# Kernel optimization log

Hardware: AMD Instinct MI355X
Metric: run time of the kernel (lower is better)

Reference implementation:

```python
import jax, jax.numpy as jnp
import numpy as np

N_NODES = 100000
N_EDGES = 50000   # number of hyperedges
NNZ = 500000      # incidence entries
IN_C = 128
OUT_C = 128


def setup_inputs() -> dict:
    key = jax.random.key(0)
    k1, k2, k3, k4 = jax.random.split(key, 4)
    x = jax.random.normal(k1, (N_NODES, IN_C), dtype=jnp.float32)
    node_idx = jax.random.randint(k2, (NNZ,), 0, N_NODES, dtype=jnp.int32)
    edge_idx = jax.random.randint(k3, (NNZ,), 0, N_EDGES, dtype=jnp.int32)
    hyperedge_index = jnp.stack([node_idx, edge_idx], axis=0)  # [2, NNZ]
    W = jax.random.normal(k4, (IN_C, OUT_C), dtype=jnp.float32) / np.sqrt(IN_C).astype(np.float32)
    b = jnp.zeros((OUT_C,), dtype=jnp.float32)
    return {"x": x, "hyperedge_index": hyperedge_index, "W": W, "b": b}


def reference(x, hyperedge_index, W, b):
    # PyG HypergraphConv (use_attention=False, heads=1, unit hyperedge weights):
    #   out = D^{-1} H B^{-1} H^T (X W) + b
    node_idx = hyperedge_index[0]  # [NNZ] node index of each incidence
    edge_idx = hyperedge_index[1]  # [NNZ] hyperedge index of each incidence

    xw = x @ W  # [N_NODES, OUT_C]

    ones = jnp.ones(node_idx.shape[0], dtype=xw.dtype)
    deg_n = jax.ops.segment_sum(ones, node_idx, num_segments=N_NODES)  # D
    d_inv = jnp.where(deg_n > 0, 1.0 / deg_n, 0.0)
    deg_e = jax.ops.segment_sum(ones, edge_idx, num_segments=N_EDGES)  # B
    b_inv = jnp.where(deg_e > 0, 1.0 / deg_e, 0.0)

    # node -> hyperedge: m_e = B^{-1}_e * sum_{v in e} xw_v
    edge_feat = jax.ops.segment_sum(xw[node_idx], edge_idx, num_segments=N_EDGES)
    edge_feat = edge_feat * b_inv[:, None]  # [N_EDGES, OUT_C]

    # hyperedge -> node: out_v = D^{-1}_v * sum_{e \ni v} m_e
    out = jax.ops.segment_sum(edge_feat[edge_idx], node_idx, num_segments=N_NODES)
    out = out * d_inv[:, None]  # [N_NODES, OUT_C]

    return out + b
```

## Files before the change

### kernel.cpp

```cpp
#include <hip/hip_runtime.h>

typedef unsigned short u16;
typedef unsigned int u32;

#define N_NODES 100000
#define N_EDGES 50000
#define C 128
#define G_GEMM 1563
#define NCNT (N_EDGES + N_NODES)
#define NBUCKC 1172
#define BCHUNK 2048

static __device__ __forceinline__ float bf2f(u16 h) {
    u32 u = ((u32)h) << 16;
    float f;
    __builtin_memcpy(&f, &u, 4);
    return f;
}

static __device__ __forceinline__ u16 f2bf(float f) {
    u32 u;
    __builtin_memcpy(&u, &f, 4);
    return (u16)((u + 0x7fffu + ((u >> 16) & 1u)) >> 16);
}

typedef short s16x8 __attribute__((ext_vector_type(8)));
typedef float f32x4 __attribute__((ext_vector_type(4)));

__global__ void transpose_w(const float* __restrict__ W, u16* __restrict__ Wt) {
    int idx = blockIdx.x * 256 + threadIdx.x;
    int k = idx >> 7, oc = idx & 127;
    Wt[oc * 128 + k] = f2bf(W[k * 128 + oc]);
}

__global__ __launch_bounds__(256) void gemm_k(
    const float* __restrict__ x, const u16* __restrict__ Wt,
    u16* __restrict__ xw) {
    __shared__ __align__(16) float xs[64 * C];
    int tid = threadIdx.x;
    int blk = blockIdx.x;
    int lane = tid & 63;
    int wave = tid >> 6;

    size_t gbase = (size_t)blk * 64 * C;
#pragma unroll
    for (int rnd = 0; rnd < 8; ++rnd) {
        int fl = rnd * 1024 + wave * 256 + lane * 4;
        int grow = blk * 64 + (fl >> 7);
        const float* src = (grow < N_NODES) ? (x + gbase + fl) : x;
        __builtin_amdgcn_global_load_lds(
            (const __attribute__((address_space(1))) void*)src,
            (__attribute__((address_space(3))) void*)(xs + rnd * 1024 + wave * 256),
            16, 0, 0);
    }
    __syncthreads();

    int tile = blk * 4 + wave;
    int m = lane & 15;
    int quad = lane >> 4;
    bool live = (tile < 6250);

    union { uint4 u; s16x8 v; } a[4];
    if (live) {
        const float* xr = xs + (wave * 16 + m) * C + quad * 8;
#pragma unroll
        for (int kk = 0; kk < 4; ++kk) {
            float4 v0 = *(const float4*)(xr + kk * 32);
            float4 v1 = *(const float4*)(xr + kk * 32 + 4);
            a[kk].u.x = (u32)f2bf(v0.x) | ((u32)f2bf(v0.y) << 16);
            a[kk].u.y = (u32)f2bf(v0.z) | ((u32)f2bf(v0.w) << 16);
            a[kk].u.z = (u32)f2bf(v1.x) | ((u32)f2bf(v1.y) << 16);
            a[kk].u.w = (u32)f2bf(v1.z) | ((u32)f2bf(v1.w) << 16);
        }
    }
    __syncthreads();

    u16* ct = (u16*)xs;
    if (live) {
        f32x4 acc[8];
#pragma unroll
        for (int nt = 0; nt < 8; ++nt) acc[nt] = (f32x4){0.f, 0.f, 0.f, 0.f};
#pragma unroll
        for (int kk = 0; kk < 4; ++kk) {
            int kb = kk * 32 + quad * 8;
#pragma unroll
            for (int nt = 0; nt < 8; ++nt) {
                union { uint4 u; s16x8 v; } b;
                b.u = *(const uint4*)(Wt + (size_t)(nt * 16 + m) * C + kb);
                acc[nt] = __builtin_amdgcn_mfma_f32_16x16x32_bf16(a[kk].v, b.v, acc[nt], 0, 0, 0);
            }
        }
#pragma unroll
        for (int nt = 0; nt < 8; ++nt)
#pragma unroll
            for (int r = 0; r < 4; ++r)
                ct[(wave * 16 + quad * 4 + r) * C + nt * 16 + m] = f2bf(acc[nt][r]);
    }
    __syncthreads();

#pragma unroll
    for (int r = 0; r < 4; ++r) {
        int f = r * 2048 + tid * 8;
        int grow = blk * 64 + (f >> 7);
        if (grow < N_NODES)
            *(uint4*)(xw + (size_t)blk * 64 * C + f) = *(const uint4*)(ct + f);
    }
}

__global__ __launch_bounds__(256) void bucket_hist_k(
    const int* __restrict__ ni, const int* __restrict__ ei,
    u32* __restrict__ cntM, int nnz, int nb1) {
    __shared__ u32 h[NBUCKC];
    for (int b = threadIdx.x; b < NBUCKC; b += 256) h[b] = 0;
    __syncthreads();
    int i0 = blockIdx.x * BCHUNK;
    int iend = min(i0 + BCHUNK, nnz);
    for (int i = i0 + threadIdx.x; i < iend; i += 256) {
        int e = ei[i], n = ni[i];
        atomicAdd(&h[e >> 7], 1u);
        atomicAdd(&h[(N_EDGES + n) >> 7], 1u);
    }
    __syncthreads();
    for (int b = threadIdx.x; b < NBUCKC; b += 256)
        cntM[(size_t)b * nb1 + blockIdx.x] = h[b];
}

__global__ __launch_bounds__(256) void scan_a2(const u32* __restrict__ cnt,
                                               u32* __restrict__ off,
                                               u32* __restrict__ bsum, int N) {
    __shared__ u32 wsum[4];
    int tid = threadIdx.x;
    int base = blockIdx.x * 1024 + tid * 4;
    u32 v0 = 0, v1 = 0, v2 = 0, v3 = 0;
    if (base + 3 < N) {
        uint4 v = *(const uint4*)(cnt + base);
        v0 = v.x; v1 = v.y; v2 = v.z; v3 = v.w;
    } else {
        if (base + 0 < N) v0 = cnt[base + 0];
        if (base + 1 < N) v1 = cnt[base + 1];
        if (base + 2 < N) v2 = cnt[base + 2];
        if (base + 3 < N) v3 = cnt[base + 3];
    }
    u32 s = v0 + v1 + v2 + v3;
    int lane = tid & 63, wv = tid >> 6;
    u32 x = s;
    for (int d = 1; d < 64; d <<= 1) {
        u32 y = __shfl_up(x, (unsigned)d);
        if (lane >= d) x += y;
    }
    if (lane == 63) wsum[wv] = x;
    __syncthreads();
    u32 wo = 0;
    for (int w = 0; w < 4; ++w) wo += (w < wv) ? wsum[w] : 0u;
    u32 ex = wo + x - s;
    if (base + 0 < N) off[base + 0] = ex;
    if (base + 1 < N) off[base + 1] = ex + v0;
    if (base + 2 < N) off[base + 2] = ex + v0 + v1;
    if (base + 3 < N) off[base + 3] = ex + v0 + v1 + v2;
    if (tid == 255) bsum[blockIdx.x] = wo + x;
}

__global__ __launch_bounds__(256) void scan_b2(u32* __restrict__ bsum, int nb) {
    __shared__ u32 wsum[4];
    int t = threadIdx.x;
    u32 v0 = (2 * t < nb) ? bsum[2 * t] : 0u;
    u32 v1 = (2 * t + 1 < nb) ? bsum[2 * t + 1] : 0u;
    u32 s = v0 + v1;
    int lane = t & 63, wv = t >> 6;
    u32 x = s;
    for (int d = 1; d < 64; d <<= 1) {
        u32 y = __shfl_up(x, (unsigned)d);
        if (lane >= d) x += y;
    }
    if (lane == 63) wsum[wv] = x;
    __syncthreads();
    u32 wo = 0;
    for (int w = 0; w < 4; ++w) wo += (w < wv) ? wsum[w] : 0u;
    u32 ex = wo + x - s;
    if (2 * t < nb) bsum[2 * t] = ex;
    if (2 * t + 1 < nb) bsum[2 * t + 1] = ex + v0;
}

__global__ __launch_bounds__(256) void bucket_place_k(
    const int* __restrict__ ni, const int* __restrict__ ei,
    const u32* __restrict__ offM, const u32* __restrict__ bsum,
    u32* __restrict__ stage, int nnz, int nb1) {
    __shared__ u32 cur[NBUCKC];
    for (int b = threadIdx.x; b < NBUCKC; b += 256) {
        size_t idx = (size_t)b * nb1 + blockIdx.x;
        cur[b] = offM[idx] + bsum[idx >> 10];
    }
    __syncthreads();
    int i0 = blockIdx.x * BCHUNK;
    int iend = min(i0 + BCHUNK, nnz);
    for (int i = i0 + threadIdx.x; i < iend; i += 256) {
        int e = ei[i], n = ni[i];
        u32 p1 = atomicAdd(&cur[e >> 7], 1u);
        stage[p1] = ((u32)(e & 127) << 17) | (u32)n;
        int k2 = N_EDGES + n;
        u32 p2 = atomicAdd(&cur[k2 >> 7], 1u);
        stage[p2] = ((u32)(k2 & 127) << 17) | (u32)e;
    }
}

__global__ __launch_bounds__(256) void bucket_csr_k(
    const u32* __restrict__ offM, const u32* __restrict__ bsum,
    const u32* __restrict__ stage, u32* __restrict__ csr,
    uint2* __restrict__ rowinfo, int nnz, int nb1) {
    __shared__ u32 h[128];
    __shared__ u32 ks[128];
    int b = blockIdx.x;
    size_t i0 = (size_t)b * nb1;
    u32 gstart = offM[i0] + bsum[i0 >> 10];
    u32 gend;
    if (b + 1 < NBUCKC) {
        size_t i1 = (size_t)(b + 1) * nb1;
        gend = offM[i1] + bsum[i1 >> 10];
    } else {
        gend = (u32)(2 * nnz);
    }
    int size = (int)(gend - gstart);
    if (threadIdx.x < 128) h[threadIdx.x] = 0;
    __syncthreads();
    for (int i = threadIdx.x; i < size; i += 256)
        atomicAdd(&h[stage[gstart + i] >> 17], 1u);
    __syncthreads();
    if (threadIdx.x < 64) {
        int l = threadIdx.x;
        u32 s0 = h[2 * l], s1 = h[2 * l + 1];
        u32 ps = s0 + s1;
        u32 x = ps;
        for (int d = 1; d < 64; d <<= 1) {
            u32 y = __shfl_up(x, (unsigned)d);
            if (l >= d) x += y;
        }
        u32 ex = x - ps;
        ks[2 * l] = ex;
        ks[2 * l + 1] = ex + s0;
        int gk = b * 128 + 2 * l;
        if (gk < NCNT) rowinfo[gk] = make_uint2(gstart + ex, s0);
        if (gk + 1 < NCNT) rowinfo[gk + 1] = make_uint2(gstart + ex + s0, s1);
    }
    __syncthreads();
    for (int i = threadIdx.x; i < size; i += 256) {
        u32 en = stage[gstart + i];
        u32 kl = en >> 17;
        u32 p = atomicAdd(&ks[kl], 1u);
        csr[gstart + p] = en & 0x1FFFFu;
    }
}

#define GATHERP(SRC)                                                          \
    for (u32 base = 0; base < deg; base += 64) {                              \
        int m = (int)min(64u, deg - base);                                    \
        int myidx = (lane < m) ? (int)csr[start + base + lane] : 0;           \
        for (int t = 0; t < m; t += 8) {                                      \
            int e0 = min(t + 0 + half, m - 1), e1 = min(t + 2 + half, m - 1); \
            int e2 = min(t + 4 + half, m - 1), e3 = min(t + 6 + half, m - 1); \
            int r0 = __shfl(myidx, e0), r1 = __shfl(myidx, e1);               \
            int r2 = __shfl(myidx, e2), r3 = __shfl(myidx, e3);               \
            uint2 u0 = ((const uint2*)(SRC + (size_t)r0 * C))[ch];            \
            uint2 u1 = ((const uint2*)(SRC + (size_t)r1 * C))[ch];            \
            uint2 u2 = ((const uint2*)(SRC + (size_t)r2 * C))[ch];            \
            uint2 u3 = ((const uint2*)(SRC + (size_t)r3 * C))[ch];            \
            float m0 = (t + 0 + half < m) ? 1.f : 0.f;                        \
            float m1 = (t + 2 + half < m) ? 1.f : 0.f;                        \
            float m2 = (t + 4 + half < m) ? 1.f : 0.f;                        \
            float m3 = (t + 6 + half < m) ? 1.f : 0.f;                        \
            a0 += m0 * bf2f((u16)(u0.x & 0xffffu)) + m1 * bf2f((u16)(u1.x & 0xffffu)) \
                + m2 * bf2f((u16)(u2.x & 0xffffu)) + m3 * bf2f((u16)(u3.x & 0xffffu)); \
            a1 += m0 * bf2f((u16)(u0.x >> 16)) + m1 * bf2f((u16)(u1.x >> 16)) \
                + m2 * bf2f((u16)(u2.x >> 16)) + m3 * bf2f((u16)(u3.x >> 16)); \
            a2 += m0 * bf2f((u16)(u0.y & 0xffffu)) + m1 * bf2f((u16)(u1.y & 0xffffu)) \
                + m2 * bf2f((u16)(u2.y & 0xffffu)) + m3 * bf2f((u16)(u3.y & 0xffffu)); \
            a3 += m0 * bf2f((u16)(u0.y >> 16)) + m1 * bf2f((u16)(u1.y >> 16)) \
                + m2 * bf2f((u16)(u2.y >> 16)) + m3 * bf2f((u16)(u3.y >> 16)); \
        }                                                                     \
    }                                                                         \
    a0 += __shfl_xor(a0, 32);                                                 \
    a1 += __shfl_xor(a1, 32);                                                 \
    a2 += __shfl_xor(a2, 32);                                                 \
    a3 += __shfl_xor(a3, 32);

__global__ __launch_bounds__(256) void edge_gather_k(const u16* __restrict__ xw,
                                                     const uint2* __restrict__ rowinfo,
                                                     const u32* __restrict__ csrC,
                                                     u16* __restrict__ ef) {
    int e = blockIdx.x * 4 + (threadIdx.x >> 6);
    if (e >= N_EDGES) return;
    int lane = threadIdx.x & 63;
    int half = lane >> 5, ch = lane & 31;
    uint2 ri = rowinfo[e];
    u32 deg = ri.y;
    u32 start = ri.x;
    const u32* csr = csrC;
    float a0 = 0.f, a1 = 0.f, a2 = 0.f, a3 = 0.f;
    GATHERP(xw)
    float sc = deg ? 1.f / (float)deg : 0.f;
    if (lane < 32) {
        uint2 w;
        w.x = (u32)f2bf(a0 * sc) | ((u32)f2bf(a1 * sc) << 16);
        w.y = (u32)f2bf(a2 * sc) | ((u32)f2bf(a3 * sc) << 16);
        ((uint2*)(ef + (size_t)e * C))[ch] = w;
    }
}

__global__ __launch_bounds__(256) void node_gather_k(const u16* __restrict__ ef,
                                                     const uint2* __restrict__ rowinfo,
                                                     const u32* __restrict__ csrC,
                                                     const float* __restrict__ bias,
                                                     float* __restrict__ out) {
    int v = blockIdx.x * 4 + (threadIdx.x >> 6);
    if (v >= N_NODES) return;
    int lane = threadIdx.x & 63;
    int half = lane >> 5, ch = lane & 31;
    uint2 ri = rowinfo[N_EDGES + v];
    u32 deg = ri.y;
    u32 start = ri.x;
    const u32* csr = csrC;
    float a0 = 0.f, a1 = 0.f, a2 = 0.f, a3 = 0.f;
    GATHERP(ef)
    float sc = deg ? 1.f / (float)deg : 0.f;
    if (lane < 32) {
        float4 bv = *(const float4*)(bias + ch * 4);
        float4 w;
        w.x = a0 * sc + bv.x;
        w.y = a1 * sc + bv.y;
        w.z = a2 * sc + bv.z;
        w.w = a3 * sc + bv.w;
        ((float4*)(out + (size_t)v * C))[ch] = w;
    }
}

extern "C" void kernel_launch(void* const* d_in, const int* in_sizes, int n_in,
                              void* d_out, int out_size, void* d_ws, size_t ws_size,
                              hipStream_t stream) {
    const float* x = (const float*)d_in[0];
    const int* node_idx = (const int*)d_in[1];
    const int nnz = in_sizes[1] / 2;
    const int* edge_idx = node_idx + nnz;
    const float* W = (const float*)d_in[2];
    const float* bias = (const float*)d_in[3];
    float* out = (float*)d_out;

    int nb1 = (nnz + BCHUNK - 1) / BCHUNK;
    int scanN = NBUCKC * nb1;
    int scanBlocks = (scanN + 1023) / 1024;

    u16* Wt = (u16*)d_ws;
    u16* ef = Wt + 16384;
    u32* cntM = (u32*)(ef + (size_t)N_EDGES * C);
    u32* offM = cntM + scanN;
    u32* bsum2 = offM + scanN;
    uint2* rowinfo = (uint2*)(bsum2 + 512);
    u32* csrC = (u32*)(rowinfo + NCNT);

    u16* xw = (u16*)d_out;
    u32* stage = (u32*)((char*)d_out + (size_t)N_NODES * C * 2);

    transpose_w<<<64, 256, 0, stream>>>(W, Wt);
    gemm_k<<<G_GEMM, 256, 0, stream>>>(x, Wt, xw);
    bucket_hist_k<<<nb1, 256, 0, stream>>>(node_idx, edge_idx, cntM, nnz, nb1);
    scan_a2<<<scanBlocks, 256, 0, stream>>>(cntM, offM, bsum2, scanN);
    scan_b2<<<1, 256, 0, stream>>>(bsum2, scanBlocks);
    bucket_place_k<<<nb1, 256, 0, stream>>>(node_idx, edge_idx, offM, bsum2,
                                            stage, nnz, nb1);
    bucket_csr_k<<<NBUCKC, 256, 0, stream>>>(offM, bsum2, stage, csrC, rowinfo,
                                             nnz, nb1);
    edge_gather_k<<<(N_EDGES + 3) / 4, 256, 0, stream>>>(xw, rowinfo, csrC, ef);
    node_gather_k<<<(N_NODES + 3) / 4, 256, 0, stream>>>(ef, rowinfo, csrC, bias, out);
}
```

Measured before the change: 212.9 us.

## Fuse weight transpose with bucket histogram and make GEMM persistent double-buffered

Merges the W transpose into the bucket histogram kernel, which removes one launch. The GEMM becomes a persistent kernel of 512 blocks that loops over row chunks. It double-buffers the x tile in LDS, prefetching the next chunk with async global-to-LDS loads while the current one computes. It also writes bf16 results straight to global memory instead of staging them through LDS, so the stores are less coalesced, and the doubled LDS use may lower occupancy.

Result: no change. 214.6 us (+0.8%).

```diff
diff --git a/kernel.cpp b/kernel.cpp
--- a/kernel.cpp
+++ b/kernel.cpp
@@ -6,7 +6,8 @@
 #define N_NODES 100000
 #define N_EDGES 50000
 #define C 128
-#define G_GEMM 1563
+#define G_CHUNK 1563
+#define GEMM_BLOCKS 512
 #define NCNT (N_EDGES + N_NODES)
 #define NBUCKC 1172
 #define BCHUNK 2048
@@ -27,93 +28,21 @@
 typedef short s16x8 __attribute__((ext_vector_type(8)));
 typedef float f32x4 __attribute__((ext_vector_type(4)));
 
-__global__ void transpose_w(const float* __restrict__ W, u16* __restrict__ Wt) {
-    int idx = blockIdx.x * 256 + threadIdx.x;
-    int k = idx >> 7, oc = idx & 127;
-    Wt[oc * 128 + k] = f2bf(W[k * 128 + oc]);
-}
-
-__global__ __launch_bounds__(256) void gemm_k(
-    const float* __restrict__ x, const u16* __restrict__ Wt,
-    u16* __restrict__ xw) {
-    __shared__ __align__(16) float xs[64 * C];
-    int tid = threadIdx.x;
-    int blk = blockIdx.x;
-    int lane = tid & 63;
-    int wave = tid >> 6;
-
-    size_t gbase = (size_t)blk * 64 * C;
-#pragma unroll
-    for (int rnd = 0; rnd < 8; ++rnd) {
-        int fl = rnd * 1024 + wave * 256 + lane * 4;
-        int grow = blk * 64 + (fl >> 7);
-        const float* src = (grow < N_NODES) ? (x + gbase + fl) : x;
-        __builtin_amdgcn_global_load_lds(
-            (const __attribute__((address_space(1))) void*)src,
-            (__attribute__((address_space(3))) void*)(xs + rnd * 1024 + wave * 256),
-            16, 0, 0);
-    }
-    __syncthreads();
-
-    int tile = blk * 4 + wave;
-    int m = lane & 15;
-    int quad = lane >> 4;
-    bool live = (tile < 6250);
-
-    union { uint4 u; s16x8 v; } a[4];
-    if (live) {
-        const float* xr = xs + (wave * 16 + m) * C + quad * 8;
-#pragma unroll
-        for (int kk = 0; kk < 4; ++kk) {
-            float4 v0 = *(const float4*)(xr + kk * 32);
-            float4 v1 = *(const float4*)(xr + kk * 32 + 4);
-            a[kk].u.x = (u32)f2bf(v0.x) | ((u32)f2bf(v0.y) << 16);
-            a[kk].u.y = (u32)f2bf(v0.z) | ((u32)f2bf(v0.w) << 16);
-            a[kk].u.z = (u32)f2bf(v1.x) | ((u32)f2bf(v1.y) << 16);
-            a[kk].u.w = (u32)f2bf(v1.z) | ((u32)f2bf(v1.w) << 16);
-        }
-    }
-    __syncthreads();
-
-    u16* ct = (u16*)xs;
-    if (live) {
-        f32x4 acc[8];
-#pragma unroll
-        for (int nt = 0; nt < 8; ++nt) acc[nt] = (f32x4){0.f, 0.f, 0.f, 0.f};
-#pragma unroll
-        for (int kk = 0; kk < 4; ++kk) {
-            int kb = kk * 32 + quad * 8;
-#pragma unroll
-            for (int nt = 0; nt < 8; ++nt) {
-                union { uint4 u; s16x8 v; } b;
-                b.u = *(const uint4*)(Wt + (size_t)(nt * 16 + m) * C + kb);
-                acc[nt] = __builtin_amdgcn_mfma_f32_16x16x32_bf16(a[kk].v, b.v, acc[nt], 0, 0, 0);
-            }
-        }
-#pragma unroll
-        for (int nt = 0; nt < 8; ++nt)
-#pragma unroll
-            for (int r = 0; r < 4; ++r)
-                ct[(wave * 16 + quad * 4 + r) * C + nt * 16 + m] = f2bf(acc[nt][r]);
-    }
-    __syncthreads();
-
-#pragma unroll
-    for (int r = 0; r < 4; ++r) {
-        int f = r * 2048 + tid * 8;
-        int grow = blk * 64 + (f >> 7);
-        if (grow < N_NODES)
-            *(uint4*)(xw + (size_t)blk * 64 * C + f) = *(const uint4*)(ct + f);
-    }
-}
-
-__global__ __launch_bounds__(256) void bucket_hist_k(
+__global__ __launch_bounds__(256) void prep_k(
+    const float* __restrict__ W, u16* __restrict__ Wt,
     const int* __restrict__ ni, const int* __restrict__ ei,
     u32* __restrict__ cntM, int nnz, int nb1) {
     __shared__ u32 h[NBUCKC];
+    if (blockIdx.x < 64) {
+        int idx = blockIdx.x * 256 + threadIdx.x;
+        int k = idx >> 7, oc = idx & 127;
+        Wt[oc * 128 + k] = f2bf(W[k * 128 + oc]);
+        return;
+    }
+    int blk = blockIdx.x - 64;
     for (int b = threadIdx.x; b < NBUCKC; b += 256) h[b] = 0;
     __syncthreads();
-    int i0 = blockIdx.x * BCHUNK;
+    int i0 = blk * BCHUNK;
     int iend = min(i0 + BCHUNK, nnz);
     for (int i = i0 + threadIdx.x; i < iend; i += 256) {
         int e = ei[i], n = ni[i];
@@ -122,7 +51,89 @@
     }
     __syncthreads();
     for (int b = threadIdx.x; b < NBUCKC; b += 256)
-        cntM[(size_t)b * nb1 + blockIdx.x] = h[b];
+        cntM[(size_t)b * nb1 + blk] = h[b];
+}
+
+__global__ __launch_bounds__(256) void gemm_k(
+    const float* __restrict__ x, const u16* __restrict__ Wt,
+    u16* __restrict__ xw) {
+    __shared__ __align__(16) float xs[2][64 * C];
+    const int tid = threadIdx.x;
+    const int lane = tid & 63;
+    const int wave = tid >> 6;
+    const int blk = blockIdx.x;
+
+    auto STAGE = [&](int c, int b) {
+        size_t gbase = (size_t)c * 64 * C;
+#pragma unroll
+        for (int rnd = 0; rnd < 8; ++rnd) {
+            int fl = rnd * 1024 + wave * 256 + lane * 4;
+            int grow = c * 64 + (fl >> 7);
+            const float* src = (grow < N_NODES) ? (x + gbase + fl) : x;
+            __builtin_amdgcn_global_load_lds(
+                (const __attribute__((address_space(1))) void*)src,
+                (__attribute__((address_space(3))) void*)(&xs[b][rnd * 1024 + wave * 256]),
+                16, 0, 0);
+        }
+    };
+
+    STAGE(blk, 0);
+    int it = 0;
+    for (int c = blk; c < G_CHUNK; c += GEMM_BLOCKS, ++it) {
+        const int cb = it & 1;
+        const int cn = c + GEMM_BLOCKS;
+        if (cn < G_CHUNK) STAGE(cn, cb ^ 1);
+        __builtin_amdgcn_sched_barrier(0);
+        asm volatile("s_waitcnt vmcnt(8)" ::: "memory");
+        __builtin_amdgcn_s_barrier();
+        __builtin_amdgcn_sched_barrier(0);
+
+        const int tile = c * 4 + wave;
+        const int m = lane & 15;
+        const int quad = lane >> 4;
+        const bool live = (tile < 6250);
+
+        union { uint4 u; s16x8 v; } a[4];
+        if (live) {
+            const float* xr = &xs[cb][(wave * 16 + m) * C + quad * 8];
+#pragma unroll
+            for (int kk = 0; kk < 4; ++kk) {
+                float4 v0 = *(const float4*)(xr + kk * 32);
+                float4 v1 = *(const float4*)(xr + kk * 32 + 4);
+                a[kk].u.x = (u32)f2bf(v0.x) | ((u32)f2bf(v0.y) << 16);
+                a[kk].u.y = (u32)f2bf(v0.z) | ((u32)f2bf(v0.w) << 16);
+                a[kk].u.z = (u32)f2bf(v1.x) | ((u32)f2bf(v1.y) << 16);
+                a[kk].u.w = (u32)f2bf(v1.z) | ((u32)f2bf(v1.w) << 16);
+            }
+        }
+        __builtin_amdgcn_sched_barrier(0);
+        __builtin_amdgcn_s_barrier();
+        __builtin_amdgcn_sched_barrier(0);
+
+        if (live) {
+            f32x4 acc[8];
+#pragma unroll
+            for (int nt = 0; nt < 8; ++nt) acc[nt] = (f32x4){0.f, 0.f, 0.f, 0.f};
+#pragma unroll
+            for (int kk = 0; kk < 4; ++kk) {
+                int kb = kk * 32 + quad * 8;
+#pragma unroll
+                for (int nt = 0; nt < 8; ++nt) {
+                    union { uint4 u; s16x8 v; } b;
+                    b.u = *(const uint4*)(Wt + (size_t)(nt * 16 + m) * C + kb);
+                    acc[nt] = __builtin_amdgcn_mfma_f32_16x16x32_bf16(
+                        a[kk].v, b.v, acc[nt], 0, 0, 0);
+                }
+            }
+            int row0 = tile * 16;
+#pragma unroll
+            for (int nt = 0; nt < 8; ++nt)
+#pragma unroll
+                for (int r = 0; r < 4; ++r)
+                    xw[(size_t)(row0 + quad * 4 + r) * C + nt * 16 + m] =
+                        f2bf(acc[nt][r]);
+        }
+    }
 }
 
 __global__ __launch_bounds__(256) void scan_a2(const u32* __restrict__ cnt,
@@ -358,9 +369,8 @@
     u16* xw = (u16*)d_out;
     u32* stage = (u32*)((char*)d_out + (size_t)N_NODES * C * 2);
 
-    transpose_w<<<64, 256, 0, stream>>>(W, Wt);
-    gemm_k<<<G_GEMM, 256, 0, stream>>>(x, Wt, xw);
-    bucket_hist_k<<<nb1, 256, 0, stream>>>(node_idx, edge_idx, cntM, nnz, nb1);
+    prep_k<<<64 + nb1, 256, 0, stream>>>(W, Wt, node_idx, edge_idx, cntM, nnz, nb1);
+    gemm_k<<<GEMM_BLOCKS, 256, 0, stream>>>(x, Wt, xw);
     scan_a2<<<scanBlocks, 256, 0, stream>>>(cntM, offM, bsum2, scanN);
     scan_b2<<<1, 256, 0, stream>>>(bsum2, scanBlocks);
     bucket_place_k<<<nb1, 256, 0, stream>>>(node_idx, edge_idx, offM, bsum2,
```

## Reorder GEMM after node-to-edge aggregation to shrink matmul to edge rows

Applied to the files above, without the earlier changes.

Uses linearity to aggregate raw fp32 x rows into hyperedges first, then applies W on the 50k edge rows instead of the 100k node rows. This removes the full node GEMM and its bf16 xw write, and also fuses the W transpose into the histogram kernel to save a launch. In exchange the edge gather now reads fp32 x rows, twice the bytes per gathered row compared with bf16 xw. Rounding also changes, since the sum is converted to bf16 before the matmul rather than after.

Result: faster. 208.5 us (-2.1%).

```diff
diff --git a/kernel.cpp b/kernel.cpp
--- a/kernel.cpp
+++ b/kernel.cpp
@@ -6,7 +6,6 @@
 #define N_NODES 100000
 #define N_EDGES 50000
 #define C 128
-#define G_GEMM 1563
 #define NCNT (N_EDGES + N_NODES)
 #define NBUCKC 1172
 #define BCHUNK 2048
@@ -27,93 +26,21 @@
 typedef short s16x8 __attribute__((ext_vector_type(8)));
 typedef float f32x4 __attribute__((ext_vector_type(4)));
 
-__global__ void transpose_w(const float* __restrict__ W, u16* __restrict__ Wt) {
-    int idx = blockIdx.x * 256 + threadIdx.x;
-    int k = idx >> 7, oc = idx & 127;
-    Wt[oc * 128 + k] = f2bf(W[k * 128 + oc]);
-}
-
-__global__ __launch_bounds__(256) void gemm_k(
-    const float* __restrict__ x, const u16* __restrict__ Wt,
-    u16* __restrict__ xw) {
-    __shared__ __align__(16) float xs[64 * C];
-    int tid = threadIdx.x;
-    int blk = blockIdx.x;
-    int lane = tid & 63;
-    int wave = tid >> 6;
-
-    size_t gbase = (size_t)blk * 64 * C;
-#pragma unroll
-    for (int rnd = 0; rnd < 8; ++rnd) {
-        int fl = rnd * 1024 + wave * 256 + lane * 4;
-        int grow = blk * 64 + (fl >> 7);
-        const float* src = (grow < N_NODES) ? (x + gbase + fl) : x;
-        __builtin_amdgcn_global_load_lds(
-            (const __attribute__((address_space(1))) void*)src,
-            (__attribute__((address_space(3))) void*)(xs + rnd * 1024 + wave * 256),
-            16, 0, 0);
-    }
-    __syncthreads();
-
-    int tile = blk * 4 + wave;
-    int m = lane & 15;
-    int quad = lane >> 4;
-    bool live = (tile < 6250);
-
-    union { uint4 u; s16x8 v; } a[4];
-    if (live) {
-        const float* xr = xs + (wave * 16 + m) * C + quad * 8;
-#pragma unroll
-        for (int kk = 0; kk < 4; ++kk) {
-            float4 v0 = *(const float4*)(xr + kk * 32);
-            float4 v1 = *(const float4*)(xr + kk * 32 + 4);
-            a[kk].u.x = (u32)f2bf(v0.x) | ((u32)f2bf(v0.y) << 16);
-            a[kk].u.y = (u32)f2bf(v0.z) | ((u32)f2bf(v0.w) << 16);
-            a[kk].u.z = (u32)f2bf(v1.x) | ((u32)f2bf(v1.y) << 16);
-            a[kk].u.w = (u32)f2bf(v1.z) | ((u32)f2bf(v1.w) << 16);
-        }
-    }
-    __syncthreads();
-
-    u16* ct = (u16*)xs;
-    if (live) {
-        f32x4 acc[8];
-#pragma unroll
-        for (int nt = 0; nt < 8; ++nt) acc[nt] = (f32x4){0.f, 0.f, 0.f, 0.f};
-#pragma unroll
-        for (int kk = 0; kk < 4; ++kk) {
-            int kb = kk * 32 + quad * 8;
-#pragma unroll
-            for (int nt = 0; nt < 8; ++nt) {
-                union { uint4 u; s16x8 v; } b;
-                b.u = *(const uint4*)(Wt + (size_t)(nt * 16 + m) * C + kb);
-                acc[nt] = __builtin_amdgcn_mfma_f32_16x16x32_bf16(a[kk].v, b.v, acc[nt], 0, 0, 0);
-            }
-        }
-#pragma unroll
-        for (int nt = 0; nt < 8; ++nt)
-#pragma unroll
-            for (int r = 0; r < 4; ++r)
-                ct[(wave * 16 + quad * 4 + r) * C + nt * 16 + m] = f2bf(acc[nt][r]);
-    }
-    __syncthreads();
-
-#pragma unroll
-    for (int r = 0; r < 4; ++r) {
-        int f = r * 2048 + tid * 8;
-        int grow = blk * 64 + (f >> 7);
-        if (grow < N_NODES)
-            *(uint4*)(xw + (size_t)blk * 64 * C + f) = *(const uint4*)(ct + f);
-    }
-}
-
-__global__ __launch_bounds__(256) void bucket_hist_k(
+__global__ __launch_bounds__(256) void prep_k(
+    const float* __restrict__ W, u16* __restrict__ Wt,
     const int* __restrict__ ni, const int* __restrict__ ei,
     u32* __restrict__ cntM, int nnz, int nb1) {
     __shared__ u32 h[NBUCKC];
+    if (blockIdx.x < 64) {
+        int idx = blockIdx.x * 256 + threadIdx.x;
+        int k = idx >> 7, oc = idx & 127;
+        Wt[oc * 128 + k] = f2bf(W[k * 128 + oc]);
+        return;
+    }
+    int blk = blockIdx.x - 64;
     for (int b = threadIdx.x; b < NBUCKC; b += 256) h[b] = 0;
     __syncthreads();
-    int i0 = blockIdx.x * BCHUNK;
+    int i0 = blk * BCHUNK;
     int iend = min(i0 + BCHUNK, nnz);
     for (int i = i0 + threadIdx.x; i < iend; i += 256) {
         int e = ei[i], n = ni[i];
@@ -122,7 +49,7 @@
     }
     __syncthreads();
     for (int b = threadIdx.x; b < NBUCKC; b += 256)
-        cntM[(size_t)b * nb1 + blockIdx.x] = h[b];
+        cntM[(size_t)b * nb1 + blk] = h[b];
 }
 
 __global__ __launch_bounds__(256) void scan_a2(const u32* __restrict__ cnt,
@@ -250,42 +177,10 @@
     }
 }
 
-#define GATHERP(SRC)                                                          \
-    for (u32 base = 0; base < deg; base += 64) {                              \
-        int m = (int)min(64u, deg - base);                                    \
-        int myidx = (lane < m) ? (int)csr[start + base + lane] : 0;           \
-        for (int t = 0; t < m; t += 8) {                                      \
-            int e0 = min(t + 0 + half, m - 1), e1 = min(t + 2 + half, m - 1); \
-            int e2 = min(t + 4 + half, m - 1), e3 = min(t + 6 + half, m - 1); \
-            int r0 = __shfl(myidx, e0), r1 = __shfl(myidx, e1);               \
-            int r2 = __shfl(myidx, e2), r3 = __shfl(myidx, e3);               \
-            uint2 u0 = ((const uint2*)(SRC + (size_t)r0 * C))[ch];            \
-            uint2 u1 = ((const uint2*)(SRC + (size_t)r1 * C))[ch];            \
-            uint2 u2 = ((const uint2*)(SRC + (size_t)r2 * C))[ch];            \
-            uint2 u3 = ((const uint2*)(SRC + (size_t)r3 * C))[ch];            \
-            float m0 = (t + 0 + half < m) ? 1.f : 0.f;                        \
-            float m1 = (t + 2 + half < m) ? 1.f : 0.f;                        \
-            float m2 = (t + 4 + half < m) ? 1.f : 0.f;                        \
-            float m3 = (t + 6 + half < m) ? 1.f : 0.f;                        \
-            a0 += m0 * bf2f((u16)(u0.x & 0xffffu)) + m1 * bf2f((u16)(u1.x & 0xffffu)) \
-                + m2 * bf2f((u16)(u2.x & 0xffffu)) + m3 * bf2f((u16)(u3.x & 0xffffu)); \
-            a1 += m0 * bf2f((u16)(u0.x >> 16)) + m1 * bf2f((u16)(u1.x >> 16)) \
-                + m2 * bf2f((u16)(u2.x >> 16)) + m3 * bf2f((u16)(u3.x >> 16)); \
-            a2 += m0 * bf2f((u16)(u0.y & 0xffffu)) + m1 * bf2f((u16)(u1.y & 0xffffu)) \
-                + m2 * bf2f((u16)(u2.y & 0xffffu)) + m3 * bf2f((u16)(u3.y & 0xffffu)); \
-            a3 += m0 * bf2f((u16)(u0.y >> 16)) + m1 * bf2f((u16)(u1.y >> 16)) \
-                + m2 * bf2f((u16)(u2.y >> 16)) + m3 * bf2f((u16)(u3.y >> 16)); \
-        }                                                                     \
-    }                                                                         \
-    a0 += __shfl_xor(a0, 32);                                                 \
-    a1 += __shfl_xor(a1, 32);                                                 \
-    a2 += __shfl_xor(a2, 32);                                                 \
-    a3 += __shfl_xor(a3, 32);
-
-__global__ __launch_bounds__(256) void edge_gather_k(const u16* __restrict__ xw,
+__global__ __launch_bounds__(256) void edge_gather_x(const float* __restrict__ x,
                                                      const uint2* __restrict__ rowinfo,
                                                      const u32* __restrict__ csrC,
-                                                     u16* __restrict__ ef) {
+                                                     u16* __restrict__ G) {
     int e = blockIdx.x * 4 + (threadIdx.x >> 6);
     if (e >= N_EDGES) return;
     int lane = threadIdx.x & 63;
@@ -293,15 +188,81 @@
     uint2 ri = rowinfo[e];
     u32 deg = ri.y;
     u32 start = ri.x;
-    const u32* csr = csrC;
     float a0 = 0.f, a1 = 0.f, a2 = 0.f, a3 = 0.f;
-    GATHERP(xw)
+    for (u32 base = 0; base < deg; base += 64) {
+        int m = (int)min(64u, deg - base);
+        int myidx = (lane < m) ? (int)csrC[start + base + lane] : 0;
+        for (int t = 0; t < m; t += 8) {
+            int e0 = min(t + 0 + half, m - 1), e1 = min(t + 2 + half, m - 1);
+            int e2 = min(t + 4 + half, m - 1), e3 = min(t + 6 + half, m - 1);
+            int r0 = __shfl(myidx, e0), r1 = __shfl(myidx, e1);
+            int r2 = __shfl(myidx, e2), r3 = __shfl(myidx, e3);
+            float4 v0 = ((const float4*)(x + (size_t)r0 * C))[ch];
+            float4 v1 = ((const float4*)(x + (size_t)r1 * C))[ch];
+            float4 v2 = ((const float4*)(x + (size_t)r2 * C))[ch];
+            float4 v3 = ((const float4*)(x + (size_t)r3 * C))[ch];
+            float m0 = (t + 0 + half < m) ? 1.f : 0.f;
+            float m1 = (t + 2 + half < m) ? 1.f : 0.f;
+            float m2 = (t + 4 + half < m) ? 1.f : 0.f;
+            float m3 = (t + 6 + half < m) ? 1.f : 0.f;
+            a0 += m0 * v0.x + m1 * v1.x + m2 * v2.x + m3 * v3.x;
+            a1 += m0 * v0.y + m1 * v1.y + m2 * v2.y + m3 * v3.y;
+            a2 += m0 * v0.z + m1 * v1.z + m2 * v2.z + m3 * v3.z;
+            a3 += m0 * v0.w + m1 * v1.w + m2 * v2.w + m3 * v3.w;
+        }
+    }
+    a0 += __shfl_xor(a0, 32);
+    a1 += __shfl_xor(a1, 32);
+    a2 += __shfl_xor(a2, 32);
+    a3 += __shfl_xor(a3, 32);
     float sc = deg ? 1.f / (float)deg : 0.f;
     if (lane < 32) {
         uint2 w;
         w.x = (u32)f2bf(a0 * sc) | ((u32)f2bf(a1 * sc) << 16);
         w.y = (u32)f2bf(a2 * sc) | ((u32)f2bf(a3 * sc) << 16);
-        ((uint2*)(ef + (size_t)e * C))[ch] = w;
+        ((uint2*)(G + (size_t)e * C))[ch] = w;
+    }
+}
+
+__global__ __launch_bounds__(256) void gemm_e(
+    const u16* __restrict__ G, const u16* __restrict__ Wt,
+    u16* __restrict__ ef) {
+    int wave = threadIdx.x >> 6;
+    int tile = blockIdx.x * 4 + wave;
+    if (tile >= 3125) return;
+    int lane = threadIdx.x & 63;
+    int m = lane & 15;
+    int quad = lane >> 4;
+    int row0 = tile * 16;
+
+    const u16* gr = G + (size_t)(row0 + m) * C + quad * 8;
+    union { uint4 u; s16x8 v; } a[4];
+#pragma unroll
+    for (int kk = 0; kk < 4; ++kk)
+        a[kk].u = *(const uint4*)(gr + kk * 32);
+
+    f32x4 acc[8];
+#pragma unroll
+    for (int nt = 0; nt < 8; ++nt) acc[nt] = (f32x4){0.f, 0.f, 0.f, 0.f};
+
+#pragma unroll
+    for (int kk = 0; kk < 4; ++kk) {
+        int kb = kk * 32 + quad * 8;
+#pragma unroll
+        for (int nt = 0; nt < 8; ++nt) {
+            union { uint4 u; s16x8 v; } b;
+            b.u = *(const uint4*)(Wt + (size_t)(nt * 16 + m) * C + kb);
+            acc[nt] = __builtin_amdgcn_mfma_f32_16x16x32_bf16(a[kk].v, b.v, acc[nt], 0, 0, 0);
+        }
+    }
+
+#pragma unroll
+    for (int nt = 0; nt < 8; ++nt) {
+#pragma unroll
+        for (int r = 0; r < 4; ++r) {
+            int row = row0 + quad * 4 + r;
+            ef[(size_t)row * C + nt * 16 + m] = f2bf(acc[nt][r]);
+        }
     }
 }
 
@@ -317,9 +278,37 @@
     uint2 ri = rowinfo[N_EDGES + v];
     u32 deg = ri.y;
     u32 start = ri.x;
-    const u32* csr = csrC;
     float a0 = 0.f, a1 = 0.f, a2 = 0.f, a3 = 0.f;
-    GATHERP(ef)
+    for (u32 base = 0; base < deg; base += 64) {
+        int m = (int)min(64u, deg - base);
+        int myidx = (lane < m) ? (int)csrC[start + base + lane] : 0;
+        for (int t = 0; t < m; t += 8) {
+            int e0 = min(t + 0 + half, m - 1), e1 = min(t + 2 + half, m - 1);
+            int e2 = min(t + 4 + half, m - 1), e3 = min(t + 6 + half, m - 1);
+            int r0 = __shfl(myidx, e0), r1 = __shfl(myidx, e1);
+            int r2 = __shfl(myidx, e2), r3 = __shfl(myidx, e3);
+            uint2 u0 = ((const uint2*)(ef + (size_t)r0 * C))[ch];
+            uint2 u1 = ((const uint2*)(ef + (size_t)r1 * C))[ch];
+            uint2 u2 = ((const uint2*)(ef + (size_t)r2 * C))[ch];
+            uint2 u3 = ((const uint2*)(ef + (size_t)r3 * C))[ch];
+            float m0 = (t + 0 + half < m) ? 1.f : 0.f;
+            float m1 = (t + 2 + half < m) ? 1.f : 0.f;
+            float m2 = (t + 4 + half < m) ? 1.f : 0.f;
+            float m3 = (t + 6 + half < m) ? 1.f : 0.f;
+            a0 += m0 * bf2f((u16)(u0.x & 0xffffu)) + m1 * bf2f((u16)(u1.x & 0xffffu))
+                + m2 * bf2f((u16)(u2.x & 0xffffu)) + m3 * bf2f((u16)(u3.x & 0xffffu));
+            a1 += m0 * bf2f((u16)(u0.x >> 16)) + m1 * bf2f((u16)(u1.x >> 16))
+                + m2 * bf2f((u16)(u2.x >> 16)) + m3 * bf2f((u16)(u3.x >> 16));
+            a2 += m0 * bf2f((u16)(u0.y & 0xffffu)) + m1 * bf2f((u16)(u1.y & 0xffffu))
+                + m2 * bf2f((u16)(u2.y & 0xffffu)) + m3 * bf2f((u16)(u3.y & 0xffffu));
+            a3 += m0 * bf2f((u16)(u0.y >> 16)) + m1 * bf2f((u16)(u1.y >> 16))
+                + m2 * bf2f((u16)(u2.y >> 16)) + m3 * bf2f((u16)(u3.y >> 16));
+        }
+    }
+    a0 += __shfl_xor(a0, 32);
+    a1 += __shfl_xor(a1, 32);
+    a2 += __shfl_xor(a2, 32);
+    a3 += __shfl_xor(a3, 32);
     float sc = deg ? 1.f / (float)deg : 0.f;
     if (lane < 32) {
         float4 bv = *(const float4*)(bias + ch * 4);
@@ -355,18 +344,17 @@
     uint2* rowinfo = (uint2*)(bsum2 + 512);
     u32* csrC = (u32*)(rowinfo + NCNT);
 
-    u16* xw = (u16*)d_out;
+    u16* G = (u16*)d_out;
     u32* stage = (u32*)((char*)d_out + (size_t)N_NODES * C * 2);
 
-    transpose_w<<<64, 256, 0, stream>>>(W, Wt);
-    gemm_k<<<G_GEMM, 256, 0, stream>>>(x, Wt, xw);
-    bucket_hist_k<<<nb1, 256, 0, stream>>>(node_idx, edge_idx, cntM, nnz, nb1);
+    prep_k<<<64 + nb1, 256, 0, stream>>>(W, Wt, node_idx, edge_idx, cntM, nnz, nb1);
     scan_a2<<<scanBlocks, 256, 0, stream>>>(cntM, offM, bsum2, scanN);
     scan_b2<<<1, 256, 0, stream>>>(bsum2, scanBlocks);
     bucket_place_k<<<nb1, 256, 0, stream>>>(node_idx, edge_idx, offM, bsum2,
                                             stage, nnz, nb1);
     bucket_csr_k<<<NBUCKC, 256, 0, stream>>>(offM, bsum2, stage, csrC, rowinfo,
                                              nnz, nb1);
-    edge_gather_k<<<(N_EDGES + 3) / 4, 256, 0, stream>>>(xw, rowinfo, csrC, ef);
+    edge_gather_x<<<(N_EDGES + 3) / 4, 256, 0, stream>>>(x, rowinfo, csrC, G);
+    gemm_e<<<(3125 + 3) / 4, 256, 0, stream>>>(G, Wt, ef);
     node_gather_k<<<(N_NODES + 3) / 4, 256, 0, stream>>>(ef, rowinfo, csrC, bias, out);
 }
```
